# Optimization experiments

Hardware: AMD Instinct MI355X
Metric: run time of the kernel (lower is better)

The kernel has to match this reference:

```python
import jax, jax.numpy as jnp
import numpy as np

# Module hyperparameters (from init_kwargs)
LEARNING_RATE = 0.01  # not used inside compute_weight_update
TAU_PLUS = 20.0
TAU_MINUS = 20.0
A_PLUS = 0.005
A_MINUS = 0.00525
TARGET_RATE = 0.1
HOMEOSTATIC_RATE = 0.001
TAU_HOMEOSTATIC = 1000.0

B, T, N_PRE, N_POST = 16, 8192, 128, 128


def setup_inputs() -> dict:
    key = jax.random.key(0)
    k1, k2, k3 = jax.random.split(key, 3)
    # Bernoulli spike trains at ~target_rate firing probability
    pre_spikes = (jax.random.uniform(k1, (B, T, N_PRE)) < TARGET_RATE).astype(jnp.float32)
    post_spikes = (jax.random.uniform(k2, (B, T, N_POST)) < TARGET_RATE).astype(jnp.float32)
    weights = jax.random.uniform(k3, (N_PRE, N_POST), dtype=jnp.float32)
    return {"pre_spikes": pre_spikes, "post_spikes": post_spikes, "weights": weights, "dt": 1}


def _temporal_corr(x, kernel, pad):
    """Correlate x [B,T,N] along time with 1-D kernel [L], padding pad=(lo,hi)."""
    b, t, n = x.shape
    xr = jnp.moveaxis(x, 1, 2).reshape(b * n, 1, t)  # [B*N, 1, T]
    k = kernel.reshape(1, 1, -1).astype(x.dtype)
    y = jax.lax.conv_general_dilated(
        xr, k, window_strides=(1,), padding=[pad],
        dimension_numbers=("NCH", "OIH", "NCH"))
    return jnp.moveaxis(y.reshape(b, n, t), 2, 1)  # [B,T,N]


def reference(pre_spikes, post_spikes, weights, dt):
    b, t, n_pre = pre_spikes.shape
    dt = float(dt)

    # Homeostatic rate tracking (first call: avg rates initialized to target_rate)
    alpha = dt / TAU_HOMEOSTATIC
    current_post_rate = post_spikes.mean(axis=(0, 1))
    avg_post_rate = (1.0 - alpha) * TARGET_RATE + alpha * current_post_rate

    # Truncated exponential STDP window: tau in 1..min(int(3*tau)-1, ...) = 1..59
    L = int(TAU_PLUS * 3)  # 60 taps (tau=0 tap zeroed)
    taus = jnp.arange(L, dtype=jnp.float32)
    w_plus = jnp.where(taus > 0, A_PLUS * jnp.exp(-taus * dt / TAU_PLUS), 0.0)
    w_minus = jnp.where(taus > 0, A_MINUS * jnp.exp(-taus * dt / TAU_MINUS), 0.0)

    # LTP: post_filt[t] = sum_{tau>=1} w_plus[tau] * post[t+tau] (future, zero-padded)
    post_filt = _temporal_corr(post_spikes, w_plus, (0, L - 1))
    # LTD: pre_filt[t] = sum_{tau>=1} w_minus[tau] * pre[t-tau] (past, zero-padded)
    pre_filt = _temporal_corr(pre_spikes, w_minus[::-1], (L - 1, 0))

    # sum_t mean_b outer(pre[t], post_filt[t]) - outer(pre_filt[t], post[t]), then /T
    ltp = jnp.einsum("btp,btq->pq", pre_spikes, post_filt)
    ltd = jnp.einsum("btp,btq->pq", pre_filt, post_spikes)
    stdp_update = (ltp - ltd) / (b * t)

    # Homeostatic regulation pulls post rate toward target
    post_rate_error = avg_post_rate - TARGET_RATE
    homeostatic_update = -HOMEOSTATIC_RATE * post_rate_error[None, :] * weights

    return stdp_update + homeostatic_update
```

## Files before the change

### kernel.cpp

```cpp
#include <hip/hip_runtime.h>

#define BB 16
#define TT 8192
#define NN 128
constexpr int CHUNK = 256;
constexpr int NCH   = BB * TT / CHUNK;
constexpr int NBLK  = NCH / 2;
constexpr int OUTN  = NN * NN;
constexpr int GS    = 264;
constexpr int SLOTS = OUTN / 2;
constexpr int PROWS = 315;

typedef _Float16 f16x8 __attribute__((ext_vector_type(8)));
typedef _Float16 f16x2 __attribute__((ext_vector_type(2)));
typedef float    f32x4 __attribute__((ext_vector_type(4)));

__device__ __forceinline__ unsigned short h16(float x) {
    _Float16 h = (_Float16)x;
    return __builtin_bit_cast(unsigned short, h);
}
__device__ __forceinline__ unsigned int pack2(float x, float y) {
    return (unsigned int)h16(x) | ((unsigned int)h16(y) << 16);
}
__device__ __forceinline__ float2 ldL(const unsigned short* p_lds, int m, int q0) {
    const unsigned int v = *(const unsigned int*)&p_lds[m * NN + q0];
    const f16x2 h = __builtin_bit_cast(f16x2, v);
    return make_float2((float)h[0], (float)h[1]);
}

template<bool ATOMIC>
__global__ __launch_bounds__(512, 2)
void stdp_main(const float* __restrict__ pre, const float* __restrict__ post,
               const int* __restrict__ dtp,
               unsigned int* __restrict__ part, float* __restrict__ wpost,
               float* __restrict__ outat)
{
    __shared__ __align__(16) unsigned short bufP[PROWS * NN];
    __shared__ __align__(16) unsigned short bufG[NN * GS];
    __shared__ float lds_ps[8 * NN];

    const int tid    = threadIdx.x;
    const int bi     = blockIdx.x;
    const int c0g    = bi * 2;
    const int b      = c0g >> 5;
    const int chunk0 = c0g & 31;
    const int t00    = chunk0 * CHUNK;
    const int t01    = t00 + CHUNK;
    const int wv     = tid >> 6;
    const int lane   = tid & 63;

    const float dtf = (float)(*dtp);
    const float r   = expf(-dtf * (1.0f / 20.0f));

    const float* pb = post + (size_t)b * TT * NN;
    const float* ab = pre  + (size_t)b * TT * NN;

    const int sc = tid & 31;
    const int mr = tid >> 5;

    for (int m = mr; m < PROWS; m += 16) {
        const int t = t00 + 1 + m;
        const float4 v = *(const float4*)(pb + (size_t)t * NN + sc * 4);
        *(uint2*)&bufP[m * NN + sc * 4] = make_uint2(pack2(v.x, v.y), pack2(v.z, v.w));
    }
    __syncthreads();

    float4 va[20];
    #pragma unroll
    for (int i = 0; i < 20; ++i) {
        const int m = mr + i * 16;
        const int t = t01 + 1 + m;
        va[i] = make_float4(0.f, 0.f, 0.f, 0.f);
        if (m < PROWS && t < TT) va[i] = *(const float4*)(pb + (size_t)t * NN + sc * 4);
    }

    const int q0 = lane * 2;

    unsigned int pk0[16], pk1[16];
    float ps0, ps1;
    #define FILTER_PHASE(SRC) {                                               \
        const int base = wv * 32;                                             \
        ps0 = 0.f; ps1 = 0.f;                                                 \
        float2 p  = ldL(SRC, base + 31, q0);                                  \
        float wt  = r;                                                        \
        float gx = r * p.x, gy = r * p.y;                                     \
        ps0 += p.x; ps1 += p.y;                                               \
        _Pragma("unroll")                                                     \
        for (int tau = 2; tau <= 59; ++tau) {                                 \
            wt *= r;                                                          \
            p = ldL(SRC, base + 30 + tau, q0);                                \
            gx = fmaf(wt, p.x, gx);                                           \
            gy = fmaf(wt, p.y, gy);                                           \
        }                                                                     \
        const float r60 = wt * r;                                             \
        pk0[15] = (unsigned int)h16(gx) << 16;                                \
        pk1[15] = (unsigned int)h16(gy) << 16;                                \
        _Pragma("unroll")                                                     \
        for (int c = 30; c >= 0; --c) {                                       \
            const float2 p1  = ldL(SRC, base + c,      q0);                   \
            const float2 p60 = ldL(SRC, base + c + 59, q0);                   \
            gx = r * (gx + p1.x) - r60 * p60.x;                               \
            gy = r * (gy + p1.y) - r60 * p60.y;                               \
            ps0 += p1.x; ps1 += p1.y;                                         \
            if (c & 1) {                                                      \
                pk0[c >> 1] = (unsigned int)h16(gx) << 16;                    \
                pk1[c >> 1] = (unsigned int)h16(gy) << 16;                    \
            } else {                                                          \
                pk0[c >> 1] |= h16(gx);                                       \
                pk1[c >> 1] |= h16(gy);                                       \
            }                                                                 \
        }                                                                     \
    }
    #define DUMP_G() {                                                        \
        unsigned short* d0 = &bufG[q0 * GS + wv * 32];                        \
        unsigned short* d1 = &bufG[(q0 + 1) * GS + wv * 32];                  \
        _Pragma("unroll")                                                     \
        for (int s = 0; s < 4; ++s) {                                         \
            *(uint4*)(d0 + 8*s) = make_uint4(pk0[4*s], pk0[4*s+1], pk0[4*s+2], pk0[4*s+3]); \
            *(uint4*)(d1 + 8*s) = make_uint4(pk1[4*s], pk1[4*s+1], pk1[4*s+2], pk1[4*s+3]); \
        }                                                                     \
        lds_ps[wv * NN + q0]     = ps0;                                       \
        lds_ps[wv * NN + q0 + 1] = ps1;                                       \
    }

    FILTER_PHASE(bufP)
    DUMP_G()
    __syncthreads();

    #pragma unroll
    for (int i = 0; i < 20; ++i) {
        const int m = mr + i * 16;
        if (m < PROWS)
            *(uint2*)&bufP[m * NN + sc * 4] =
                make_uint2(pack2(va[i].x, va[i].y), pack2(va[i].z, va[i].w));
    }

    if (tid < NN) {
        float s = 0.f;
        #pragma unroll
        for (int w = 0; w < 8; ++w) s += lds_ps[w * NN + tid];
        if (chunk0 == 0) s += pb[tid];
        if constexpr (ATOMIC) atomicAdd(&wpost[tid], s);
        else wpost[(size_t)tid * NCH + c0g] = s;
    }

    const int pr0 = wv * 16;
    f32x4 acc[8];
    #pragma unroll
    for (int qt = 0; qt < 8; ++qt) acc[qt] = (f32x4){0.f, 0.f, 0.f, 0.f};

    #define MFMA_PHASE(T0) {                                                  \
        const float* abase = ab + (size_t)((T0) + (lane >> 4) * 8) * NN + pr0 + (lane & 15); \
        float an[8];                                                          \
        _Pragma("unroll")                                                     \
        for (int j = 0; j < 8; ++j) an[j] = abase[(size_t)j * NN];            \
        _Pragma("unroll")                                                     \
        for (int ks = 0; ks < 8; ++ks) {                                      \
            f16x8 af;                                                         \
            _Pragma("unroll")                                                 \
            for (int j = 0; j < 8; ++j) af[j] = (_Float16)an[j];              \
            if (ks < 7) {                                                     \
                const float* src = abase + (size_t)((ks + 1) * 32) * NN;      \
                _Pragma("unroll")                                             \
                for (int j = 0; j < 8; ++j) an[j] = src[(size_t)j * NN];      \
            }                                                                 \
            const int koff = ks * 32 + (lane >> 4) * 8;                       \
            _Pragma("unroll")                                                 \
            for (int qt = 0; qt < 8; ++qt) {                                  \
                const f16x8 bf = *(const f16x8*)&bufG[(qt * 16 + (lane & 15)) * GS + koff]; \
                acc[qt] = __builtin_amdgcn_mfma_f32_16x16x32_f16(af, bf, acc[qt], 0, 0, 0); \
            }                                                                 \
        }                                                                     \
    }

    MFMA_PHASE(t00)
    __syncthreads();

    FILTER_PHASE(bufP)
    DUMP_G()
    __syncthreads();

    if (tid < NN) {
        float s = 0.f;
        #pragma unroll
        for (int w = 0; w < 8; ++w) s += lds_ps[w * NN + tid];
        if constexpr (ATOMIC) atomicAdd(&wpost[tid], s);
        else wpost[(size_t)tid * NCH + c0g + 1] = s;
    }

    MFMA_PHASE(t01)

    if constexpr (!ATOMIC) {
        unsigned int* dst = part + ((size_t)bi * 8 + wv) * 1024 + lane;
        #pragma unroll
        for (int qt = 0; qt < 8; ++qt)
            #pragma unroll
            for (int rp = 0; rp < 2; ++rp)
                dst[qt * 128 + rp * 64] = pack2(acc[qt][2 * rp], acc[qt][2 * rp + 1]);
    } else {
        #pragma unroll
        for (int qt = 0; qt < 8; ++qt)
            #pragma unroll
            for (int rg = 0; rg < 4; ++rg) {
                const int prow = pr0 + (lane >> 4) * 4 + rg;
                const int qcol = qt * 16 + (lane & 15);
                atomicAdd(&outat[prow * NN + qcol], acc[qt][rg]);
            }
    }
    #undef FILTER_PHASE
    #undef DUMP_G
    #undef MFMA_PHASE
}

__global__ __launch_bounds__(512)
void finalize_ws(const unsigned int* __restrict__ part, const float* __restrict__ wpost,
                 const int* __restrict__ dtp, const float* __restrict__ W,
                 float* __restrict__ out)
{
    __shared__ float2 red[512];
    __shared__ float  hfs[16];
    const int s    = threadIdx.x & 63;
    const int kq   = threadIdx.x >> 6;
    const int slot = blockIdx.x * 64 + s;
    const int qt   = (slot >> 7) & 7;
    const int qbase = qt * 16;

    {
        const int qi = threadIdx.x >> 5;
        const int pr = threadIdx.x & 31;
        float hsum = 0.f;
        const float* wq = wpost + (size_t)(qbase + qi) * NCH;
        #pragma unroll 4
        for (int k = pr; k < NCH; k += 32) hsum += wq[k];
        #pragma unroll
        for (int off = 16; off; off >>= 1) hsum += __shfl_down(hsum, off, 32);
        if (pr == 0) {
            const float dtf   = (float)(*dtp);
            const float alpha = dtf * 1e-3f;
            hfs[qi] = -0.001f * (alpha * (hsum * (1.0f / (float)(BB * TT)) - 0.1f));
        }
    }

    float sx = 0.f, sy = 0.f;
    #pragma unroll 8
    for (int k = kq * (NBLK / 8); k < (kq + 1) * (NBLK / 8); ++k) {
        const unsigned int v = part[(size_t)k * SLOTS + slot];
        const f16x2 h = __builtin_bit_cast(f16x2, v);
        sx += (float)h[0];
        sy += (float)h[1];
    }
    red[threadIdx.x] = make_float2(sx, sy);
    __syncthreads();
    if (threadIdx.x < 64) {
        float tx = red[s].x, ty = red[s].y;
        #pragma unroll
        for (int g = 1; g < 8; ++g) {
            const float2 v = red[g * 64 + s];
            tx += v.x; ty += v.y;
        }
        const int lane = slot & 63;
        const int rp   = (slot >> 6) & 1;
        const int wv   = slot >> 10;
        const int p    = wv * 16 + ((lane >> 4) << 2) + rp * 2;
        const int qi   = lane & 15;
        const int q    = qbase + qi;
        const float scale = (float)((0.005 - 0.00525) / (double)(BB * TT));
        const float hf = hfs[qi];
        out[p * NN + q]       = fmaf(tx, scale, hf * W[p * NN + q]);
        out[(p + 1) * NN + q] = fmaf(ty, scale, hf * W[(p + 1) * NN + q]);
    }
}

__global__ void finalize_at(const float* __restrict__ wpost, const int* __restrict__ dtp,
                            const float* __restrict__ W, float* __restrict__ out)
{
    const int i = (blockIdx.x * 256 + threadIdx.x) * 2;
    const int q = i & 127;
    const float scale = (float)((0.005 - 0.00525) / (double)(BB * TT));
    const float dtf   = (float)(*dtp);
    const float alpha = dtf * 1e-3f;
    const float inv   = 1.0f / (float)(BB * TT);
    const float hf0   = -0.001f * (alpha * (wpost[q]     * inv - 0.1f));
    const float hf1   = -0.001f * (alpha * (wpost[q + 1] * inv - 0.1f));
    float2 sv = *(const float2*)(out + i);
    float2 w  = *(const float2*)(W + i);
    float2 o;
    o.x = fmaf(sv.x, scale, hf0 * w.x);
    o.y = fmaf(sv.y, scale, hf1 * w.y);
    *(float2*)(out + i) = o;
}

extern "C" void kernel_launch(void* const* d_in, const int* in_sizes, int n_in,
                              void* d_out, int out_size, void* d_ws, size_t ws_size,
                              hipStream_t stream)
{
    const float* pre  = (const float*)d_in[0];
    const float* post = (const float*)d_in[1];
    const float* W    = (const float*)d_in[2];
    const int*   dtp  = (const int*)d_in[3];
    float* out = (float*)d_out;

    const size_t part_bytes  = (size_t)NBLK * SLOTS * sizeof(unsigned int);
    const size_t wpost_bytes = (size_t)NN * NCH * sizeof(float);
    const size_t need = part_bytes + wpost_bytes;

    if (ws_size >= need) {
        unsigned int* part = (unsigned int*)d_ws;
        float* wpost       = (float*)((char*)d_ws + part_bytes);
        hipLaunchKernelGGL((stdp_main<false>), dim3(NBLK), dim3(512), 0, stream,
                           pre, post, dtp, part, wpost, (float*)nullptr);
        hipLaunchKernelGGL(finalize_ws, dim3(SLOTS / 64), dim3(512), 0, stream,
                           part, wpost, dtp, W, out);
    } else {
        float* wpost = (float*)d_ws;
        hipMemsetAsync(d_out, 0, OUTN * sizeof(float), stream);
        hipMemsetAsync(wpost, 0, NN * sizeof(float), stream);
        hipLaunchKernelGGL((stdp_main<true>), dim3(NBLK), dim3(512), 0, stream,
                           pre, post, dtp, (unsigned int*)nullptr, wpost, out);
        hipLaunchKernelGGL(finalize_at, dim3(OUTN / 512), dim3(256), 0, stream,
                           wpost, dtp, W, out);
    }
}
```

Measured before the change: 162.4 us.

## Double block to 16 waves, halve filter windows and split MFMA q-tiles

Launches the main kernel with 1024 threads (16 waves), so each wave filters a 16-step window instead of 32 and computes half of the output q-tiles in the MFMA phase. The initial 59-tap exponential sum is split into four independent accumulators to shorten the serial FMA dependency chain. The goal is more wave-level parallelism and latency hiding per CU, since LDS use already limits each CU to about one block. In exchange, the 59-tap prologue is repeated twice as often per chunk, and the tighter launch bounds may cause register spills.

Result: slower. 195.0 us (+20.1%).

```diff
diff --git a/kernel.cpp b/kernel.cpp
--- a/kernel.cpp
+++ b/kernel.cpp
@@ -10,6 +10,8 @@
 constexpr int GS    = 264;
 constexpr int SLOTS = OUTN / 2;
 constexpr int PROWS = 315;
+constexpr int NWAVE = 16;
+constexpr int WIN   = CHUNK / NWAVE;
 
 typedef _Float16 f16x8 __attribute__((ext_vector_type(8)));
 typedef _Float16 f16x2 __attribute__((ext_vector_type(2)));
@@ -29,7 +31,7 @@
 }
 
 template<bool ATOMIC>
-__global__ __launch_bounds__(512, 2)
+__global__ __launch_bounds__(1024, 4)
 void stdp_main(const float* __restrict__ pre, const float* __restrict__ post,
                const int* __restrict__ dtp,
                unsigned int* __restrict__ part, float* __restrict__ wpost,
@@ -37,7 +39,7 @@
 {
     __shared__ __align__(16) unsigned short bufP[PROWS * NN];
     __shared__ __align__(16) unsigned short bufG[NN * GS];
-    __shared__ float lds_ps[8 * NN];
+    __shared__ float lds_ps[NWAVE * NN];
 
     const int tid    = threadIdx.x;
     const int bi     = blockIdx.x;
@@ -58,45 +60,61 @@
     const int sc = tid & 31;
     const int mr = tid >> 5;
 
-    for (int m = mr; m < PROWS; m += 16) {
+    for (int m = mr; m < PROWS; m += 32) {
         const int t = t00 + 1 + m;
         const float4 v = *(const float4*)(pb + (size_t)t * NN + sc * 4);
         *(uint2*)&bufP[m * NN + sc * 4] = make_uint2(pack2(v.x, v.y), pack2(v.z, v.w));
     }
     __syncthreads();
 
-    float4 va[20];
+    float4 va[10];
     #pragma unroll
-    for (int i = 0; i < 20; ++i) {
-        const int m = mr + i * 16;
+    for (int i = 0; i < 10; ++i) {
+        const int m = mr + i * 32;
         const int t = t01 + 1 + m;
         va[i] = make_float4(0.f, 0.f, 0.f, 0.f);
         if (m < PROWS && t < TT) va[i] = *(const float4*)(pb + (size_t)t * NN + sc * 4);
     }
 
-    const int q0 = lane * 2;
-
-    unsigned int pk0[16], pk1[16];
+    const int q0   = lane * 2;
+    const int base = wv * WIN;
+
+    unsigned int pk0[8], pk1[8];
     float ps0, ps1;
     #define FILTER_PHASE(SRC) {                                               \
-        const int base = wv * 32;                                             \
-        ps0 = 0.f; ps1 = 0.f;                                                 \
-        float2 p  = ldL(SRC, base + 31, q0);                                  \
-        float wt  = r;                                                        \
-        float gx = r * p.x, gy = r * p.y;                                     \
-        ps0 += p.x; ps1 += p.y;                                               \
+        const float r2 = r * r, r3 = r2 * r, r4 = r2 * r2;                    \
+        float2 p = ldL(SRC, base + 15, q0);                        \
+        ps0 = p.x; ps1 = p.y;                                                 \
+        float gx0 = r  * p.x, gy0 = r  * p.y;                                 \
+        p = ldL(SRC, base + 16, q0);                               \
+        float gx1 = r2 * p.x, gy1 = r2 * p.y;                                 \
+        p = ldL(SRC, base + 17, q0);                               \
+        float gx2 = r3 * p.x, gy2 = r3 * p.y;                                 \
+        p = ldL(SRC, base + 18, q0);                               \
+        float gx3 = r4 * p.x, gy3 = r4 * p.y;                                 \
+        float wA = r * r4, wB = r2 * r4, wC = r3 * r4, wD = r4 * r4;          \
         _Pragma("unroll")                                                     \
-        for (int tau = 2; tau <= 59; ++tau) {                                 \
-            wt *= r;                                                          \
-            p = ldL(SRC, base + 30 + tau, q0);                                \
-            gx = fmaf(wt, p.x, gx);                                           \
-            gy = fmaf(wt, p.y, gy);                                           \
+        for (int j = 1; j < 15; ++j) {                                        \
+            p = ldL(SRC, base + 15 + 4 * j, q0);                              \
+            gx0 = fmaf(wA, p.x, gx0); gy0 = fmaf(wA, p.y, gy0);               \
+            p = ldL(SRC, base + 16 + 4 * j, q0);                              \
+            gx1 = fmaf(wB, p.x, gx1); gy1 = fmaf(wB, p.y, gy1);               \
+            p = ldL(SRC, base + 17 + 4 * j, q0);                              \
+            gx2 = fmaf(wC, p.x, gx2); gy2 = fmaf(wC, p.y, gy2);               \
+            if (j < 14) {                                                     \
+                p = ldL(SRC, base + 18 + 4 * j, q0);                          \
+                gx3 = fmaf(wD, p.x, gx3); gy3 = fmaf(wD, p.y, gy3);           \
+            }                                                                 \
+            wA *= r4; wB *= r4; wC *= r4; wD *= r4;                           \
         }                                                                     \
-        const float r60 = wt * r;                                             \
-        pk0[15] = (unsigned int)h16(gx) << 16;                                \
-        pk1[15] = (unsigned int)h16(gy) << 16;                                \
+        const float r8 = r4 * r4, r16 = r8 * r8, r32 = r16 * r16;             \
+        const float r60 = ((r32 * r16) * r8) * r4;                            \
+        float gx = (gx0 + gx1) + (gx2 + gx3);                                 \
+        float gy = (gy0 + gy1) + (gy2 + gy3);                                 \
+        pk0[7] = (unsigned int)h16(gx) << 16;                                 \
+        pk1[7] = (unsigned int)h16(gy) << 16;                                 \
         _Pragma("unroll")                                                     \
-        for (int c = 30; c >= 0; --c) {                                       \
+        for (int c = 14; c >= 0; --c) {                                       \
             const float2 p1  = ldL(SRC, base + c,      q0);                   \
             const float2 p60 = ldL(SRC, base + c + 59, q0);                   \
             gx = r * (gx + p1.x) - r60 * p60.x;                               \
@@ -112,13 +130,12 @@
         }                                                                     \
     }
     #define DUMP_G() {                                                        \
-        unsigned short* d0 = &bufG[q0 * GS + wv * 32];                        \
-        unsigned short* d1 = &bufG[(q0 + 1) * GS + wv * 32];                  \
-        _Pragma("unroll")                                                     \
-        for (int s = 0; s < 4; ++s) {                                         \
-            *(uint4*)(d0 + 8*s) = make_uint4(pk0[4*s], pk0[4*s+1], pk0[4*s+2], pk0[4*s+3]); \
-            *(uint4*)(d1 + 8*s) = make_uint4(pk1[4*s], pk1[4*s+1], pk1[4*s+2], pk1[4*s+3]); \
-        }                                                                     \
+        unsigned short* d0 = &bufG[q0 * GS + base];                           \
+        unsigned short* d1 = &bufG[(q0 + 1) * GS + base];                     \
+        *(uint4*)(d0)     = make_uint4(pk0[0], pk0[1], pk0[2], pk0[3]);       \
+        *(uint4*)(d0 + 8) = make_uint4(pk0[4], pk0[5], pk0[6], pk0[7]);       \
+        *(uint4*)(d1)     = make_uint4(pk1[0], pk1[1], pk1[2], pk1[3]);       \
+        *(uint4*)(d1 + 8) = make_uint4(pk1[4], pk1[5], pk1[6], pk1[7]);       \
         lds_ps[wv * NN + q0]     = ps0;                                       \
         lds_ps[wv * NN + q0 + 1] = ps1;                                       \
     }
@@ -128,8 +145,8 @@
     __syncthreads();
 
     #pragma unroll
-    for (int i = 0; i < 20; ++i) {
-        const int m = mr + i * 16;
+    for (int i = 0; i < 10; ++i) {
+        const int m = mr + i * 32;
         if (m < PROWS)
             *(uint2*)&bufP[m * NN + sc * 4] =
                 make_uint2(pack2(va[i].x, va[i].y), pack2(va[i].z, va[i].w));
@@ -138,16 +155,17 @@
     if (tid < NN) {
         float s = 0.f;
         #pragma unroll
-        for (int w = 0; w < 8; ++w) s += lds_ps[w * NN + tid];
+        for (int w = 0; w < NWAVE; ++w) s += lds_ps[w * NN + tid];
         if (chunk0 == 0) s += pb[tid];
         if constexpr (ATOMIC) atomicAdd(&wpost[tid], s);
         else wpost[(size_t)tid * NCH + c0g] = s;
     }
 
-    const int pr0 = wv * 16;
-    f32x4 acc[8];
+    const int pr0 = (wv & 7) * 16;
+    const int qtb = (wv >> 3) * 4;
+    f32x4 acc[4];
     #pragma unroll
-    for (int qt = 0; qt < 8; ++qt) acc[qt] = (f32x4){0.f, 0.f, 0.f, 0.f};
+    for (int qi = 0; qi < 4; ++qi) acc[qi] = (f32x4){0.f, 0.f, 0.f, 0.f};
 
     #define MFMA_PHASE(T0) {                                                  \
         const float* abase = ab + (size_t)((T0) + (lane >> 4) * 8) * NN + pr0 + (lane & 15); \
@@ -166,9 +184,9 @@
             }                                                                 \
             const int koff = ks * 32 + (lane >> 4) * 8;                       \
             _Pragma("unroll")                                                 \
-            for (int qt = 0; qt < 8; ++qt) {                                  \
-                const f16x8 bf = *(const f16x8*)&bufG[(qt * 16 + (lane & 15)) * GS + koff]; \
-                acc[qt] = __builtin_amdgcn_mfma_f32_16x16x32_f16(af, bf, acc[qt], 0, 0, 0); \
+            for (int qi = 0; qi < 4; ++qi) {                                  \
+                const f16x8 bf = *(const f16x8*)&bufG[((qtb + qi) * 16 + (lane & 15)) * GS + koff]; \
+                acc[qi] = __builtin_amdgcn_mfma_f32_16x16x32_f16(af, bf, acc[qi], 0, 0, 0); \
             }                                                                 \
         }                                                                     \
     }
@@ -183,7 +201,7 @@
     if (tid < NN) {
         float s = 0.f;
         #pragma unroll
-        for (int w = 0; w < 8; ++w) s += lds_ps[w * NN + tid];
+        for (int w = 0; w < NWAVE; ++w) s += lds_ps[w * NN + tid];
         if constexpr (ATOMIC) atomicAdd(&wpost[tid], s);
         else wpost[(size_t)tid * NCH + c0g + 1] = s;
     }
@@ -191,20 +209,21 @@
     MFMA_PHASE(t01)
 
     if constexpr (!ATOMIC) {
-        unsigned int* dst = part + ((size_t)bi * 8 + wv) * 1024 + lane;
-        #pragma unroll
-        for (int qt = 0; qt < 8; ++qt)
-            #pragma unroll
-            for (int rp = 0; rp < 2; ++rp)
-                dst[qt * 128 + rp * 64] = pack2(acc[qt][2 * rp], acc[qt][2 * rp + 1]);
+        unsigned int* dst = part + ((size_t)bi * 8 + (wv & 7)) * 1024 + lane;
+        #pragma unroll
+        for (int qi = 0; qi < 4; ++qi) {
+            const int qt = qtb + qi;
+            dst[qt * 128]      = pack2(acc[qi][0], acc[qi][1]);
+            dst[qt * 128 + 64] = pack2(acc[qi][2], acc[qi][3]);
+        }
     } else {
         #pragma unroll
-        for (int qt = 0; qt < 8; ++qt)
+        for (int qi = 0; qi < 4; ++qi)
             #pragma unroll
             for (int rg = 0; rg < 4; ++rg) {
                 const int prow = pr0 + (lane >> 4) * 4 + rg;
-                const int qcol = qt * 16 + (lane & 15);
-                atomicAdd(&outat[prow * NN + qcol], acc[qt][rg]);
+                const int qcol = (qtb + qi) * 16 + (lane & 15);
+                atomicAdd(&outat[prow * NN + qcol], acc[qi][rg]);
             }
     }
     #undef FILTER_PHASE
@@ -307,7 +326,7 @@
     if (ws_size >= need) {
         unsigned int* part = (unsigned int*)d_ws;
         float* wpost       = (float*)((char*)d_ws + part_bytes);
-        hipLaunchKernelGGL((stdp_main<false>), dim3(NBLK), dim3(512), 0, stream,
+        hipLaunchKernelGGL((stdp_main<false>), dim3(NBLK), dim3(1024), 0, stream,
                            pre, post, dtp, part, wpost, (float*)nullptr);
         hipLaunchKernelGGL(finalize_ws, dim3(SLOTS / 64), dim3(512), 0, stream,
                            part, wpost, dtp, W, out);
@@ -315,7 +334,7 @@
         float* wpost = (float*)d_ws;
         hipMemsetAsync(d_out, 0, OUTN * sizeof(float), stream);
         hipMemsetAsync(wpost, 0, NN * sizeof(float), stream);
-        hipLaunchKernelGGL((stdp_main<true>), dim3(NBLK), dim3(512), 0, stream,
+        hipLaunchKernelGGL((stdp_main<true>), dim3(NBLK), dim3(1024), 0, stream,
                            pre, post, dtp, (unsigned int*)nullptr, wpost, out);
         hipLaunchKernelGGL(finalize_at, dim3(OUTN / 512), dim3(256), 0, stream,
                            wpost, dtp, W, out);
```
